# Performance work log

Measured on AMD Instinct MI355X. Metric: run time of the kernel, lower is better.

Reference implementation:

```python
import jax, jax.numpy as jnp
import numpy as np
import math

N = 100000   # nodes
E = 1600000  # edges
H = 64       # hidden_dim
TD = 32      # time_dim
B = 8        # number of graphs in batch

def _lin(key, din, dout):
    kw, kb = jax.random.split(key)
    s = 1.0 / math.sqrt(din)
    return (jax.random.uniform(kw, (din, dout), jnp.float32, -s, s),
            jax.random.uniform(kb, (dout,), jnp.float32, -s, s))

def setup_inputs() -> dict:
    key = jax.random.key(0)
    ks = jax.random.split(key, 20)
    inp = {}
    inp['condition'] = jax.random.normal(ks[0], (N, 6), jnp.float32)
    inp['edge_attr'] = jax.random.normal(ks[1], (E, 2), jnp.float32)
    inp['edge_index'] = jax.random.randint(ks[2], (2, E), 0, N, jnp.int64 if jax.config.jax_enable_x64 else jnp.int32)
    inp['batch'] = jnp.sort(jax.random.randint(ks[3], (N,), 0, B))
    # node_mlp: 7->H->H
    inp['w_n1'], inp['b_n1'] = _lin(ks[4], 7, H)
    inp['w_n2'], inp['b_n2'] = _lin(ks[5], H, H)
    # edge_mlp: 2->H->H
    inp['w_e1'], inp['b_e1'] = _lin(ks[6], 2, H)
    inp['w_e2'], inp['b_e2'] = _lin(ks[7], H, H)
    # time_mlp: SiLU -> Linear(TD,H)
    inp['w_t'], inp['b_t'] = _lin(ks[8], TD, H)
    # three GINEConv inner MLPs: H->H->H each
    inp['w_c1a'], inp['b_c1a'] = _lin(ks[9], H, H)
    inp['w_c1b'], inp['b_c1b'] = _lin(ks[10], H, H)
    inp['w_c2a'], inp['b_c2a'] = _lin(ks[11], H, H)
    inp['w_c2b'], inp['b_c2b'] = _lin(ks[12], H, H)
    inp['w_c3a'], inp['b_c3a'] = _lin(ks[13], H, H)
    inp['w_c3b'], inp['b_c3b'] = _lin(ks[14], H, H)
    # final_mlp: H->H->1
    inp['w_f1'], inp['b_f1'] = _lin(ks[15], H, H)
    inp['w_f2'], inp['b_f2'] = _lin(ks[16], H, 1)
    return inp

def _mlp2(x, w1, b1, w2, b2):
    return jax.nn.silu(x @ w1 + b1) @ w2 + b2

def _time_emb(t, dim):
    half = dim // 2
    freqs = jnp.exp(jnp.arange(half, dtype=jnp.float32) * (-math.log(10000.0) / (half - 1)))
    ang = t[:, None].astype(jnp.float32) * freqs[None, :]
    return jnp.concatenate([jnp.sin(ang), jnp.cos(ang)], axis=-1)

def _gine_conv(h, ef, src, dst, w1, b1, w2, b2):
    # GINEConv (eps=0): nn(x_i + sum_j relu(x_j + edge_attr))
    msg = jax.nn.relu(h[src] + ef)                       # [E,H]
    agg = jax.ops.segment_sum(msg, dst, num_segments=N)  # [N,H]
    return _mlp2(h + agg, w1, b1, w2, b2)

def reference(condition, edge_attr,
              w_n1, b_n1, w_n2, b_n2,
              w_e1, b_e1, w_e2, b_e2,
              w_t, b_t,
              w_c1a, b_c1a, w_c1b, b_c1b,
              w_c2a, b_c2a, w_c2b, b_c2b,
              w_c3a, b_c3a, w_c3b, b_c3b,
              w_f1, b_f1, w_f2, b_f2,
              edge_index, batch):
    n = condition.shape[0]
    x_in = jnp.concatenate([jnp.zeros((n, 1), condition.dtype), condition], axis=-1)  # [N,7]
    h = _mlp2(x_in, w_n1, b_n1, w_n2, b_n2)          # [N,H]
    ef = _mlp2(edge_attr, w_e1, b_e1, w_e2, b_e2)    # [E,H]
    # t = zeros(batch_size) as in original; batch_size = B (static)
    t_emb = _time_emb(jnp.zeros((B,), jnp.float32), TD)   # [B,TD]
    t_feat = jax.nn.silu(t_emb) @ w_t + b_t               # [B,H]
    h = h + t_feat[batch]
    src, dst = edge_index[0], edge_index[1]
    h = jax.nn.silu(_gine_conv(h, ef, src, dst, w_c1a, b_c1a, w_c1b, b_c1b))
    h = jax.nn.silu(_gine_conv(h, ef, src, dst, w_c2a, b_c2a, w_c2b, b_c2b))
    h = jax.nn.silu(_gine_conv(h, ef, src, dst, w_c3a, b_c3a, w_c3b, b_c3b))
    return _mlp2(h, w_f1, b_f1, w_f2, b_f2)          # [N,1]
```

## Files before the change

kernel.cpp:

```cpp
#include <hip/hip_runtime.h>
#include <hip/hip_bf16.h>

#define NN 100000
#define NE 1600000
#define SCAN_BLOCKS 98

typedef short short8 __attribute__((ext_vector_type(8)));
typedef float floatx4 __attribute__((ext_vector_type(4)));

__device__ __forceinline__ float silu_f(float x){ return x / (1.0f + __expf(-x)); }

__device__ __forceinline__ unsigned short f2bf(float x) {
    __hip_bfloat16 h = __float2bfloat16(x);
    unsigned short u; __builtin_memcpy(&u, &h, 2); return u;
}
__device__ __forceinline__ float bf2f(unsigned short u) {
    return __uint_as_float((unsigned)u << 16);
}

__device__ __forceinline__ float dot64(const float* vec, const float* wrow) {
    float ax = 0.f, ay = 0.f, az = 0.f, aw = 0.f;
#pragma unroll
    for (int k = 0; k < 64; k += 4) {
        float4 w = *(const float4*)(wrow + k);
        float4 v = *(const float4*)(vec + k);
        ax = fmaf(v.x, w.x, ax); ay = fmaf(v.y, w.y, ay);
        az = fmaf(v.z, w.z, az); aw = fmaf(v.w, w.w, aw);
    }
    return (ax + ay) + (az + aw);
}
__device__ __forceinline__ void load_wT(const float* __restrict__ w, float* s, int t) {
    for (int i = t; i < 4096; i += 256) { int k = i >> 6, j = i & 63; s[j * 68 + k] = w[i]; }
}

__global__ void tvec_kernel(const float* __restrict__ w_t, const float* __restrict__ b_t,
                            float* __restrict__ tvec) {
    int j = threadIdx.x;
    const float s1 = 0.7310585786300049f;
    float acc = b_t[j];
#pragma unroll
    for (int i = 16; i < 32; ++i) acc = fmaf(s1, w_t[i * 64 + j], acc);
    tvec[j] = acc;
}

__global__ __launch_bounds__(256) void node_init_kernel(
    const float* __restrict__ cond,
    const float* __restrict__ w1, const float* __restrict__ b1,
    const float* __restrict__ w2, const float* __restrict__ b2,
    const float* __restrict__ tvec,
    float* __restrict__ h, float* __restrict__ agg)
{
    __shared__ float s_w1[6 * 64];
    __shared__ float s_w2t[64 * 68];
    __shared__ float s_b1[64], s_b2[64];
    __shared__ float s_hid[4][64];
    int t = threadIdx.x;
    for (int i = t; i < 384; i += 256) s_w1[i] = w1[64 + i];
    load_wT(w2, s_w2t, t);
    if (t < 64) { s_b1[t] = b1[t]; s_b2[t] = b2[t] + tvec[t]; }
    __syncthreads();
    int lane = t & 63, grp = t >> 6;
    const int groups = (NN + 3) >> 2;
    for (int g = blockIdx.x; g < groups; g += gridDim.x) {
        int n = (g << 2) + grp;
        if (n < NN) {
            float acc = s_b1[lane];
#pragma unroll
            for (int i = 0; i < 6; ++i) acc = fmaf(cond[n * 6 + i], s_w1[i * 64 + lane], acc);
            s_hid[grp][lane] = silu_f(acc);
            float o = s_b2[lane] + dot64(s_hid[grp], s_w2t + lane * 68);
            size_t off = (size_t)n * 64 + lane;
            h[off] = o;
            if (agg) agg[off] = 0.f;
        }
    }
}

__global__ __launch_bounds__(256) void zero_kernel(int* __restrict__ p, int n) {
    int i = blockIdx.x * 256 + threadIdx.x;
    if (i < n) p[i] = 0;
}
__global__ __launch_bounds__(256) void hist_kernel(const int* __restrict__ dst, int* __restrict__ cnt) {
    int e = blockIdx.x * 256 + threadIdx.x;
    if (e < NE) atomicAdd(&cnt[dst[e]], 1);
}
__global__ __launch_bounds__(256) void scan1_kernel(const int* __restrict__ cnt,
                                                    int* __restrict__ offs, int* __restrict__ bsum) {
    __shared__ int s_w[4];
    int t = threadIdx.x;
    int base = blockIdx.x * 1024 + t * 4;
    int v0 = (base + 0 < NN) ? cnt[base + 0] : 0;
    int v1 = (base + 1 < NN) ? cnt[base + 1] : 0;
    int v2 = (base + 2 < NN) ? cnt[base + 2] : 0;
    int v3 = (base + 3 < NN) ? cnt[base + 3] : 0;
    int tsum = v0 + v1 + v2 + v3;
    int lane = t & 63, w = t >> 6;
    int x = tsum;
#pragma unroll
    for (int d = 1; d < 64; d <<= 1) { int y = __shfl_up(x, d, 64); if (lane >= d) x += y; }
    if (lane == 63) s_w[w] = x;
    __syncthreads();
    if (t == 0) {
        int a = 0;
#pragma unroll
        for (int i = 0; i < 4; ++i) { int b = s_w[i]; s_w[i] = a; a += b; }
        bsum[blockIdx.x] = a;
    }
    __syncthreads();
    int excl = x - tsum + s_w[w];
    if (base + 0 < NN) offs[base + 0] = excl;
    if (base + 1 < NN) offs[base + 1] = excl + v0;
    if (base + 2 < NN) offs[base + 2] = excl + v0 + v1;
    if (base + 3 < NN) offs[base + 3] = excl + v0 + v1 + v2;
}
__global__ void scan2_kernel(const int* __restrict__ bsum, int* __restrict__ bscan, int nb) {
    __shared__ int s_w[2];
    int t = threadIdx.x;
    int v = (t < nb) ? bsum[t] : 0;
    int lane = t & 63, w = t >> 6;
    int x = v;
#pragma unroll
    for (int d = 1; d < 64; d <<= 1) { int y = __shfl_up(x, d, 64); if (lane >= d) x += y; }
    if (lane == 63) s_w[w] = x;
    __syncthreads();
    int add = (w == 1) ? s_w[0] : 0;
    if (t < nb) bscan[t] = x - v + add;
}
__global__ __launch_bounds__(256) void scan3_kernel(int* __restrict__ offs,
                                                    const int* __restrict__ bscan,
                                                    int* __restrict__ cursor) {
    int i = blockIdx.x * 256 + threadIdx.x;
    if (i < NN) {
        int v = offs[i] + bscan[i >> 10];
        offs[i] = v;
        cursor[i] = v;
    }
    if (i == 0) offs[NN] = NE;
}
__global__ __launch_bounds__(256) void scatter_pack_kernel(const int* __restrict__ dst,
                                                           const int* __restrict__ src,
                                                           const float* __restrict__ ea,
                                                           int* __restrict__ cursor,
                                                           int4* __restrict__ pack) {
    int e = blockIdx.x * 256 + threadIdx.x;
    if (e >= NE) return;
    float2 a = *(const float2*)(ea + (size_t)e * 2);
    int pos = atomicAdd(&cursor[dst[e]], 1);
    pack[pos] = make_int4(src[e], __float_as_int(a.x), __float_as_int(a.y), 0);
}
__global__ __launch_bounds__(256) void copy_src_kernel(const int4* __restrict__ pack,
                                                       int* __restrict__ srcc) {
    int i = blockIdx.x * 256 + threadIdx.x;
    if (i < NE) srcc[i] = pack[i].x;
}

__global__ __launch_bounds__(256, 2) void edge_feat_mfma_kernel(
    const int4* __restrict__ pack,
    const float* __restrict__ w1, const float* __restrict__ b1,
    const float* __restrict__ w2, const float* __restrict__ b2,
    __hip_bfloat16* __restrict__ ef)
{
    int t = threadIdx.x;
    int lane = t & 63, wv = t >> 6;
    int er = lane & 15;
    int kg = lane >> 4;
    float w1x[2][8], w1y[2][8], b1v[2][8];
#pragma unroll
    for (int c = 0; c < 2; ++c)
#pragma unroll
        for (int j = 0; j < 8; ++j) {
            int k = c * 32 + kg * 8 + j;
            w1x[c][j] = w1[k];
            w1y[c][j] = w1[64 + k];
            b1v[c][j] = b1[k];
        }
    short8 bfrag[2][4];
#pragma unroll
    for (int c = 0; c < 2; ++c)
#pragma unroll
        for (int tt = 0; tt < 4; ++tt)
#pragma unroll
            for (int j = 0; j < 8; ++j) {
                int k = c * 32 + kg * 8 + j;
                bfrag[c][tt][j] = (short)f2bf(w2[k * 64 + 4 * er + tt]);
            }
    float4 b2v = *(const float4*)(b2 + 4 * er);

    const int nchunk = NE / 16;
    for (int ch = blockIdx.x * 4 + wv; ch < nchunk; ch += gridDim.x * 4) {
        int i0 = ch * 16;
        int4 p = pack[i0 + er];
        float ax = __int_as_float(p.y), ay = __int_as_float(p.z);
        short8 afrag[2];
#pragma unroll
        for (int c = 0; c < 2; ++c)
#pragma unroll
            for (int j = 0; j < 8; ++j) {
                float hid = silu_f(fmaf(ax, w1x[c][j], fmaf(ay, w1y[c][j], b1v[c][j])));
                afrag[c][j] = (short)f2bf(hid);
            }
        floatx4 acc0 = {0,0,0,0}, acc1 = {0,0,0,0}, acc2 = {0,0,0,0}, acc3 = {0,0,0,0};
        acc0 = __builtin_amdgcn_mfma_f32_16x16x32_bf16(afrag[0], bfrag[0][0], acc0, 0, 0, 0);
        acc0 = __builtin_amdgcn_mfma_f32_16x16x32_bf16(afrag[1], bfrag[1][0], acc0, 0, 0, 0);
        acc1 = __builtin_amdgcn_mfma_f32_16x16x32_bf16(afrag[0], bfrag[0][1], acc1, 0, 0, 0);
        acc1 = __builtin_amdgcn_mfma_f32_16x16x32_bf16(afrag[1], bfrag[1][1], acc1, 0, 0, 0);
        acc2 = __builtin_amdgcn_mfma_f32_16x16x32_bf16(afrag[0], bfrag[0][2], acc2, 0, 0, 0);
        acc2 = __builtin_amdgcn_mfma_f32_16x16x32_bf16(afrag[1], bfrag[1][2], acc2, 0, 0, 0);
        acc3 = __builtin_amdgcn_mfma_f32_16x16x32_bf16(afrag[0], bfrag[0][3], acc3, 0, 0, 0);
        acc3 = __builtin_amdgcn_mfma_f32_16x16x32_bf16(afrag[1], bfrag[1][3], acc3, 0, 0, 0);
#pragma unroll
        for (int q = 0; q < 4; ++q) {
            ushort4 o;
            o.x = f2bf(acc0[q] + b2v.x);
            o.y = f2bf(acc1[q] + b2v.y);
            o.z = f2bf(acc2[q] + b2v.z);
            o.w = f2bf(acc3[q] + b2v.w);
            *(ushort4*)((unsigned short*)ef + (size_t)(i0 + kg * 4 + q) * 64 + 4 * er) = o;
        }
    }
}

__global__ __launch_bounds__(256) void agg_kernel(
    const float* __restrict__ hin, float* __restrict__ u,
    const int* __restrict__ offs, const int* __restrict__ srcc,
    const __hip_bfloat16* __restrict__ ef)
{
    int t = threadIdx.x, lane = t & 63, grp = t >> 6;
    int n = blockIdx.x * 4 + grp;
    if (n >= NN) return;
    size_t off = (size_t)n * 64 + lane;
    float acc = hin[off];
    const unsigned short* efu = (const unsigned short*)ef;
    int i0 = offs[n], i1 = offs[n + 1];
    for (int ib = i0; ib < i1; ib += 64) {
        int m = i1 - ib; if (m > 64) m = 64;
        int myS = 0;
        if (lane < m) myS = srcc[ib + lane];
        int j = 0;
        for (; j + 8 <= m; j += 8) {
            float hs[8], ev[8];
#pragma unroll
            for (int q = 0; q < 8; ++q) {
                int s = __shfl(myS, j + q, 64);
                hs[q] = hin[(size_t)s * 64 + lane];
                ev[q] = __uint_as_float((unsigned)efu[(size_t)(ib + j + q) * 64 + lane] << 16);
            }
#pragma unroll
            for (int q = 0; q < 8; ++q) acc += fmaxf(hs[q] + ev[q], 0.f);
        }
        for (; j < m; ++j) {
            int s = __shfl(myS, j, 64);
            float hs = hin[(size_t)s * 64 + lane];
            float ev = __uint_as_float((unsigned)efu[(size_t)(ib + j) * 64 + lane] << 16);
            acc += fmaxf(hs + ev, 0.f);
        }
    }
    u[off] = acc;
}

__global__ __launch_bounds__(256) void node_mlp_mfma_kernel(
    const float* __restrict__ u, float* __restrict__ h,
    const float* __restrict__ wa, const float* __restrict__ ba,
    const float* __restrict__ wb, const float* __restrict__ bb)
{
    __shared__ float s_hid[4][16 * 72];
    int t = threadIdx.x, lane = t & 63, wv = t >> 6;
    int er = lane & 15, kg = lane >> 4;
    short8 waH[2][4], waL[2][4], wbH[2][4], wbL[2][4];
#pragma unroll
    for (int c = 0; c < 2; ++c)
#pragma unroll
        for (int tt = 0; tt < 4; ++tt)
#pragma unroll
            for (int j = 0; j < 8; ++j) {
                int k = c * 32 + kg * 8 + j;
                float vA = wa[k * 64 + 4 * er + tt];
                unsigned short hA = f2bf(vA);
                waH[c][tt][j] = (short)hA;
                waL[c][tt][j] = (short)f2bf(vA - bf2f(hA));
                float vB = wb[k * 64 + 4 * er + tt];
                unsigned short hB = f2bf(vB);
                wbH[c][tt][j] = (short)hB;
                wbL[c][tt][j] = (short)f2bf(vB - bf2f(hB));
            }
    float4 bav = *(const float4*)(ba + 4 * er);
    float4 bbv = *(const float4*)(bb + 4 * er);
    float* hid = s_hid[wv];

    const int ntile = NN / 16;
    for (int tile = blockIdx.x * 4 + wv; tile < ntile; tile += gridDim.x * 4) {
        int i0 = tile * 16;
        short8 aH[2], aL[2];
#pragma unroll
        for (int c = 0; c < 2; ++c) {
            const float* up = u + (size_t)(i0 + er) * 64 + c * 32 + kg * 8;
            float4 u0 = *(const float4*)(up);
            float4 u1 = *(const float4*)(up + 4);
            float uv[8] = {u0.x, u0.y, u0.z, u0.w, u1.x, u1.y, u1.z, u1.w};
#pragma unroll
            for (int j = 0; j < 8; ++j) {
                unsigned short hi = f2bf(uv[j]);
                aH[c][j] = (short)hi;
                aL[c][j] = (short)f2bf(uv[j] - bf2f(hi));
            }
        }
        floatx4 acc[4] = {{0,0,0,0},{0,0,0,0},{0,0,0,0},{0,0,0,0}};
#pragma unroll
        for (int tt = 0; tt < 4; ++tt)
#pragma unroll
            for (int c = 0; c < 2; ++c) {
                acc[tt] = __builtin_amdgcn_mfma_f32_16x16x32_bf16(aH[c], waH[c][tt], acc[tt], 0, 0, 0);
                acc[tt] = __builtin_amdgcn_mfma_f32_16x16x32_bf16(aL[c], waH[c][tt], acc[tt], 0, 0, 0);
                acc[tt] = __builtin_amdgcn_mfma_f32_16x16x32_bf16(aH[c], waL[c][tt], acc[tt], 0, 0, 0);
            }
#pragma unroll
        for (int q = 0; q < 4; ++q) {
            float4 hv;
            hv.x = silu_f(acc[0][q] + bav.x);
            hv.y = silu_f(acc[1][q] + bav.y);
            hv.z = silu_f(acc[2][q] + bav.z);
            hv.w = silu_f(acc[3][q] + bav.w);
            *(float4*)(hid + (kg * 4 + q) * 72 + 4 * er) = hv;
        }
        short8 cH[2], cL[2];
#pragma unroll
        for (int c = 0; c < 2; ++c) {
            const float* hp = hid + er * 72 + c * 32 + kg * 8;
            float4 h0 = *(const float4*)(hp);
            float4 h1 = *(const float4*)(hp + 4);
            float hv[8] = {h0.x, h0.y, h0.z, h0.w, h1.x, h1.y, h1.z, h1.w};
#pragma unroll
            for (int j = 0; j < 8; ++j) {
                unsigned short hi = f2bf(hv[j]);
                cH[c][j] = (short)hi;
                cL[c][j] = (short)f2bf(hv[j] - bf2f(hi));
            }
        }
        floatx4 acc2[4] = {{0,0,0,0},{0,0,0,0},{0,0,0,0},{0,0,0,0}};
#pragma unroll
        for (int tt = 0; tt < 4; ++tt)
#pragma unroll
            for (int c = 0; c < 2; ++c) {
                acc2[tt] = __builtin_amdgcn_mfma_f32_16x16x32_bf16(cH[c], wbH[c][tt], acc2[tt], 0, 0, 0);
                acc2[tt] = __builtin_amdgcn_mfma_f32_16x16x32_bf16(cL[c], wbH[c][tt], acc2[tt], 0, 0, 0);
                acc2[tt] = __builtin_amdgcn_mfma_f32_16x16x32_bf16(cH[c], wbL[c][tt], acc2[tt], 0, 0, 0);
            }
#pragma unroll
        for (int q = 0; q < 4; ++q) {
            float4 ov;
            ov.x = silu_f(acc2[0][q] + bbv.x);
            ov.y = silu_f(acc2[1][q] + bbv.y);
            ov.z = silu_f(acc2[2][q] + bbv.z);
            ov.w = silu_f(acc2[3][q] + bbv.w);
            *(float4*)(h + (size_t)(i0 + kg * 4 + q) * 64 + 4 * er) = ov;
        }
    }
}

__global__ __launch_bounds__(256, 3) void edge_feat_fallback_kernel(
    const float* __restrict__ ea,
    const float* __restrict__ w1, const float* __restrict__ b1,
    const float* __restrict__ w2, const float* __restrict__ b2,
    __hip_bfloat16* __restrict__ ef)
{
    __shared__ float s_w1[128], s_b1[64], s_b2[64];
    __shared__ float s_hid[4][64];
    int t = threadIdx.x;
    if (t < 128) s_w1[t] = w1[t];
    if (t < 64) { s_b1[t] = b1[t]; s_b2[t] = b2[t]; }
    int lane = t & 63, grp = t >> 6;
    __syncthreads();
    const int groups = NE >> 2;
    for (int g = blockIdx.x; g < groups; g += gridDim.x) {
        int e = (g << 2) + grp;
        float2 a = *(const float2*)(ea + (size_t)e * 2);
        float acc = fmaf(a.x, s_w1[lane], fmaf(a.y, s_w1[64 + lane], s_b1[lane]));
        s_hid[grp][lane] = silu_f(acc);
        float o = s_b2[lane];
#pragma unroll
        for (int k = 0; k < 64; k += 4) {
            float4 v = *(const float4*)&s_hid[grp][k];
            o = fmaf(v.x, w2[(k+0)*64+lane], o);
            o = fmaf(v.y, w2[(k+1)*64+lane], o);
            o = fmaf(v.z, w2[(k+2)*64+lane], o);
            o = fmaf(v.w, w2[(k+3)*64+lane], o);
        }
        ef[(size_t)e * 64 + lane] = __float2bfloat16(o);
    }
}

__global__ __launch_bounds__(256) void msg_agg_kernel(
    const int* __restrict__ src, const int* __restrict__ dst,
    const float* __restrict__ h, const __hip_bfloat16* __restrict__ ef,
    float* __restrict__ agg)
{
    int tid = blockIdx.x * 256 + threadIdx.x;
    int e = tid >> 4;
    if (e >= NE) return;
    int q = tid & 15;
    int s = src[e], d = dst[e];
    float4 hv = *(const float4*)(h + (size_t)s * 64 + q * 4);
    ushort4 ev = *(const ushort4*)(ef + (size_t)e * 64 + q * 4);
    float m0 = fmaxf(hv.x + __uint_as_float((unsigned)ev.x << 16), 0.f);
    float m1 = fmaxf(hv.y + __uint_as_float((unsigned)ev.y << 16), 0.f);
    float m2 = fmaxf(hv.z + __uint_as_float((unsigned)ev.z << 16), 0.f);
    float m3 = fmaxf(hv.w + __uint_as_float((unsigned)ev.w << 16), 0.f);
    float* ap = agg + (size_t)d * 64 + q * 4;
    atomicAdd(ap + 0, m0); atomicAdd(ap + 1, m1);
    atomicAdd(ap + 2, m2); atomicAdd(ap + 3, m3);
}

__global__ __launch_bounds__(256) void node_update_kernel(
    float* __restrict__ h, float* __restrict__ agg,
    const float* __restrict__ wa, const float* __restrict__ ba,
    const float* __restrict__ wb, const float* __restrict__ bb)
{
    __shared__ float s_wat[64 * 68], s_wbt[64 * 68];
    __shared__ float s_ba[64], s_bb[64];
    __shared__ float s_u[4][64], s_hid[4][64];
    int t = threadIdx.x;
    load_wT(wa, s_wat, t);
    load_wT(wb, s_wbt, t);
    if (t < 64) { s_ba[t] = ba[t]; s_bb[t] = bb[t]; }
    __syncthreads();
    int lane = t & 63, grp = t >> 6;
    const int groups = (NN + 3) >> 2;
    for (int g = blockIdx.x; g < groups; g += gridDim.x) {
        int n = (g << 2) + grp;
        if (n < NN) {
            size_t off = (size_t)n * 64 + lane;
            float uv = h[off] + agg[off];
            agg[off] = 0.f;
            s_u[grp][lane] = uv;
            float hid = silu_f(s_ba[lane] + dot64(s_u[grp], s_wat + lane * 68));
            s_hid[grp][lane] = hid;
            float o = silu_f(s_bb[lane] + dot64(s_hid[grp], s_wbt + lane * 68));
            h[off] = o;
        }
    }
}

__global__ __launch_bounds__(256) void final_kernel(
    const float* __restrict__ hin,
    const float* __restrict__ w1, const float* __restrict__ b1,
    const float* __restrict__ w2, const float* __restrict__ b2,
    float* __restrict__ out)
{
    __shared__ float s_w1t[64 * 68];
    __shared__ float s_b1[64], s_w2[64];
    __shared__ float s_u[4][64];
    int t = threadIdx.x;
    load_wT(w1, s_w1t, t);
    if (t < 64) { s_b1[t] = b1[t]; s_w2[t] = w2[t]; }
    __syncthreads();
    int lane = t & 63, grp = t >> 6;
    float b2v = b2[0];
    const int groups = (NN + 3) >> 2;
    for (int g = blockIdx.x; g < groups; g += gridDim.x) {
        int n = (g << 2) + grp;
        if (n < NN) {
            s_u[grp][lane] = hin[(size_t)n * 64 + lane];
            float hid = silu_f(s_b1[lane] + dot64(s_u[grp], s_w1t + lane * 68));
            float v = hid * s_w2[lane];
#pragma unroll
            for (int off = 32; off; off >>= 1) v += __shfl_xor(v, off, 64);
            if (lane == 0) out[n] = v + b2v;
        }
    }
}

extern "C" void kernel_launch(void* const* d_in, const int* in_sizes, int n_in,
                              void* d_out, int out_size, void* d_ws, size_t ws_size,
                              hipStream_t stream) {
    const float* cond = (const float*)d_in[0];
    const float* ea   = (const float*)d_in[1];
    const int*   ei   = (const int*)d_in[2];
    const float* w_n1 = (const float*)d_in[4];  const float* b_n1 = (const float*)d_in[5];
    const float* w_n2 = (const float*)d_in[6];  const float* b_n2 = (const float*)d_in[7];
    const float* w_e1 = (const float*)d_in[8];  const float* b_e1 = (const float*)d_in[9];
    const float* w_e2 = (const float*)d_in[10]; const float* b_e2 = (const float*)d_in[11];
    const float* w_t  = (const float*)d_in[12]; const float* b_t  = (const float*)d_in[13];
    const float* wca[3] = {(const float*)d_in[14], (const float*)d_in[18], (const float*)d_in[22]};
    const float* bca[3] = {(const float*)d_in[15], (const float*)d_in[19], (const float*)d_in[23]};
    const float* wcb[3] = {(const float*)d_in[16], (const float*)d_in[20], (const float*)d_in[24]};
    const float* bcb[3] = {(const float*)d_in[17], (const float*)d_in[21], (const float*)d_in[25]};
    const float* w_f1 = (const float*)d_in[26]; const float* b_f1 = (const float*)d_in[27];
    const float* w_f2 = (const float*)d_in[28]; const float* b_f2 = (const float*)d_in[29];
    float* out = (float*)d_out;

    const int* srcp = ei;
    const int* dstp = ei + NE;
    char* ws = (char*)d_ws;

    size_t o = 0;
    float* tvec = (float*)(ws + o); o += 256;
    float* h    = (float*)(ws + o); o += (size_t)NN * 64 * 4;
    float* u    = (float*)(ws + o); o += (size_t)NN * 64 * 4;
    int* offs   = (int*)(ws + o);   o += ((size_t)(NN + 1) * 4 + 255) & ~255ULL;
    int* cnt    = (int*)(ws + o);   o += ((size_t)NN * 4 + 255) & ~255ULL;
    int* bsum   = (int*)(ws + o);   o += 512;
    int* bscan  = (int*)(ws + o);   o += 512;
    int* srcc   = (int*)(ws + o);   o += (size_t)NE * 4;
    __hip_bfloat16* ef = (__hip_bfloat16*)(ws + o); o += (size_t)NE * 64 * 2;
    const size_t REQ_A = o;
    int4* pack = (int4*)u;

    if (ws_size >= REQ_A) {
        hipLaunchKernelGGL(tvec_kernel, dim3(1), dim3(64), 0, stream, w_t, b_t, tvec);
        hipLaunchKernelGGL(zero_kernel, dim3((NN + 255) / 256), dim3(256), 0, stream, cnt, NN);
        hipLaunchKernelGGL(hist_kernel, dim3((NE + 255) / 256), dim3(256), 0, stream, dstp, cnt);
        hipLaunchKernelGGL(scan1_kernel, dim3(SCAN_BLOCKS), dim3(256), 0, stream, cnt, offs, bsum);
        hipLaunchKernelGGL(scan2_kernel, dim3(1), dim3(128), 0, stream, bsum, bscan, SCAN_BLOCKS);
        hipLaunchKernelGGL(scan3_kernel, dim3((NN + 255) / 256), dim3(256), 0, stream, offs, bscan, cnt);
        hipLaunchKernelGGL(scatter_pack_kernel, dim3((NE + 255) / 256), dim3(256), 0, stream,
                           dstp, srcp, ea, cnt, pack);
        hipLaunchKernelGGL(copy_src_kernel, dim3((NE + 255) / 256), dim3(256), 0, stream,
                           pack, srcc);
        hipLaunchKernelGGL(node_init_kernel, dim3(1024), dim3(256), 0, stream,
                           cond, w_n1, b_n1, w_n2, b_n2, tvec, h, (float*)nullptr);
        hipLaunchKernelGGL(edge_feat_mfma_kernel, dim3(2048), dim3(256), 0, stream,
                           pack, w_e1, b_e1, w_e2, b_e2, ef);
        for (int l = 0; l < 3; ++l) {
            hipLaunchKernelGGL(agg_kernel, dim3((NN + 3) / 4), dim3(256), 0, stream,
                               h, u, offs, srcc, ef);
            hipLaunchKernelGGL(node_mlp_mfma_kernel, dim3(391), dim3(256), 0, stream,
                               u, h, wca[l], bca[l], wcb[l], bcb[l]);
        }
        hipLaunchKernelGGL(final_kernel, dim3(1024), dim3(256), 0, stream,
                           h, w_f1, b_f1, w_f2, b_f2, out);
    } else {
        float* tvecB = (float*)ws;
        float* hB    = (float*)(ws + 256);
        float* agg   = hB + (size_t)NN * 64;
        __hip_bfloat16* efB = (__hip_bfloat16*)(agg + (size_t)NN * 64);
        hipLaunchKernelGGL(tvec_kernel, dim3(1), dim3(64), 0, stream, w_t, b_t, tvecB);
        hipLaunchKernelGGL(node_init_kernel, dim3(1024), dim3(256), 0, stream,
                           cond, w_n1, b_n1, w_n2, b_n2, tvecB, hB, agg);
        hipLaunchKernelGGL(edge_feat_fallback_kernel, dim3(1024), dim3(256), 0, stream,
                           ea, w_e1, b_e1, w_e2, b_e2, efB);
        for (int l = 0; l < 3; ++l) {
            hipLaunchKernelGGL(msg_agg_kernel, dim3((NE * 16) / 256), dim3(256), 0, stream,
                               srcp, dstp, hB, efB, agg);
            hipLaunchKernelGGL(node_update_kernel, dim3(1024), dim3(256), 0, stream,
                               hB, agg, wca[l], bca[l], wcb[l], bcb[l]);
        }
        hipLaunchKernelGGL(final_kernel, dim3(1024), dim3(256), 0, stream,
                           hB, w_f1, b_f1, w_f2, b_f2, out);
    }
}
```

Before: 640.9 us.

## Aggregate two nodes per wavefront with paired features and nontemporal edge loads

The aggregation kernel now maps each node to a half-wavefront of 32 lanes. Each lane handles two features, using float2 gathers of h and 32-bit loads of packed bf16 edge features, so each memory instruction moves more bytes and each wave covers twice as many nodes. Edge-feature and source-index streams use nontemporal loads, and the edge MLP writes its output with nontemporal stores, so these streamed data are meant to pollute the cache less and leave room for the reused h rows. The risk is longer per-lane serial chains and more divergence between the two nodes sharing a wave when their degrees differ.

```diff
diff --git a/kernel.cpp b/kernel.cpp
--- a/kernel.cpp
+++ b/kernel.cpp
@@ -7,6 +7,8 @@
 
 typedef short short8 __attribute__((ext_vector_type(8)));
 typedef float floatx4 __attribute__((ext_vector_type(4)));
+typedef int   intx4   __attribute__((ext_vector_type(4)));
+typedef unsigned short ushortx4 __attribute__((ext_vector_type(4)));
 
 __device__ __forceinline__ float silu_f(float x){ return x / (1.0f + __expf(-x)); }
 
@@ -141,21 +143,22 @@
                                                            const int* __restrict__ src,
                                                            const float* __restrict__ ea,
                                                            int* __restrict__ cursor,
-                                                           int4* __restrict__ pack) {
+                                                           intx4* __restrict__ pack) {
     int e = blockIdx.x * 256 + threadIdx.x;
     if (e >= NE) return;
     float2 a = *(const float2*)(ea + (size_t)e * 2);
     int pos = atomicAdd(&cursor[dst[e]], 1);
-    pack[pos] = make_int4(src[e], __float_as_int(a.x), __float_as_int(a.y), 0);
-}
-__global__ __launch_bounds__(256) void copy_src_kernel(const int4* __restrict__ pack,
+    intx4 p = { src[e], __float_as_int(a.x), __float_as_int(a.y), 0 };
+    pack[pos] = p;
+}
+__global__ __launch_bounds__(256) void copy_src_kernel(const intx4* __restrict__ pack,
                                                        int* __restrict__ srcc) {
     int i = blockIdx.x * 256 + threadIdx.x;
     if (i < NE) srcc[i] = pack[i].x;
 }
 
 __global__ __launch_bounds__(256, 2) void edge_feat_mfma_kernel(
-    const int4* __restrict__ pack,
+    const intx4* __restrict__ pack,
     const float* __restrict__ w1, const float* __restrict__ b1,
     const float* __restrict__ w2, const float* __restrict__ b2,
     __hip_bfloat16* __restrict__ ef)
@@ -189,7 +192,7 @@
     const int nchunk = NE / 16;
     for (int ch = blockIdx.x * 4 + wv; ch < nchunk; ch += gridDim.x * 4) {
         int i0 = ch * 16;
-        int4 p = pack[i0 + er];
+        intx4 p = __builtin_nontemporal_load(pack + i0 + er);
         float ax = __int_as_float(p.y), ay = __int_as_float(p.z);
         short8 afrag[2];
 #pragma unroll
@@ -210,12 +213,13 @@
         acc3 = __builtin_amdgcn_mfma_f32_16x16x32_bf16(afrag[1], bfrag[1][3], acc3, 0, 0, 0);
 #pragma unroll
         for (int q = 0; q < 4; ++q) {
-            ushort4 o;
+            ushortx4 o;
             o.x = f2bf(acc0[q] + b2v.x);
             o.y = f2bf(acc1[q] + b2v.y);
             o.z = f2bf(acc2[q] + b2v.z);
             o.w = f2bf(acc3[q] + b2v.w);
-            *(ushort4*)((unsigned short*)ef + (size_t)(i0 + kg * 4 + q) * 64 + 4 * er) = o;
+            __builtin_nontemporal_store(o,
+                (ushortx4*)((unsigned short*)ef + (size_t)(i0 + kg * 4 + q) * 64 + 4 * er));
         }
     }
 }
@@ -225,37 +229,43 @@
     const int* __restrict__ offs, const int* __restrict__ srcc,
     const __hip_bfloat16* __restrict__ ef)
 {
-    int t = threadIdx.x, lane = t & 63, grp = t >> 6;
-    int n = blockIdx.x * 4 + grp;
+    int t = threadIdx.x;
+    int lane = t & 63, wv = t >> 6;
+    int half = lane >> 5, l32 = lane & 31;
+    int n = blockIdx.x * 8 + wv * 2 + half;
     if (n >= NN) return;
-    size_t off = (size_t)n * 64 + lane;
-    float acc = hin[off];
-    const unsigned short* efu = (const unsigned short*)ef;
+    size_t off = (size_t)n * 64 + l32 * 2;
+    float2 acc = *(const float2*)(hin + off);
+    const unsigned int* efu = (const unsigned int*)ef;
     int i0 = offs[n], i1 = offs[n + 1];
-    for (int ib = i0; ib < i1; ib += 64) {
-        int m = i1 - ib; if (m > 64) m = 64;
+    for (int ib = i0; ib < i1; ib += 32) {
+        int m = i1 - ib; if (m > 32) m = 32;
         int myS = 0;
-        if (lane < m) myS = srcc[ib + lane];
+        if (l32 < m) myS = __builtin_nontemporal_load(srcc + ib + l32);
         int j = 0;
         for (; j + 8 <= m; j += 8) {
-            float hs[8], ev[8];
+            float2 hs[8]; unsigned int ev[8];
 #pragma unroll
             for (int q = 0; q < 8; ++q) {
-                int s = __shfl(myS, j + q, 64);
-                hs[q] = hin[(size_t)s * 64 + lane];
-                ev[q] = __uint_as_float((unsigned)efu[(size_t)(ib + j + q) * 64 + lane] << 16);
-            }
-#pragma unroll
-            for (int q = 0; q < 8; ++q) acc += fmaxf(hs[q] + ev[q], 0.f);
+                int s = __shfl(myS, j + q, 32);
+                hs[q] = *(const float2*)(hin + (size_t)s * 64 + l32 * 2);
+                ev[q] = __builtin_nontemporal_load(efu + (size_t)(ib + j + q) * 32 + l32);
+            }
+#pragma unroll
+            for (int q = 0; q < 8; ++q) {
+                acc.x += fmaxf(hs[q].x + bf2f((unsigned short)(ev[q] & 0xffffu)), 0.f);
+                acc.y += fmaxf(hs[q].y + bf2f((unsigned short)(ev[q] >> 16)), 0.f);
+            }
         }
         for (; j < m; ++j) {
-            int s = __shfl(myS, j, 64);
-            float hs = hin[(size_t)s * 64 + lane];
-            float ev = __uint_as_float((unsigned)efu[(size_t)(ib + j) * 64 + lane] << 16);
-            acc += fmaxf(hs + ev, 0.f);
-        }
-    }
-    u[off] = acc;
+            int s = __shfl(myS, j, 32);
+            float2 hs = *(const float2*)(hin + (size_t)s * 64 + l32 * 2);
+            unsigned int ev = __builtin_nontemporal_load(efu + (size_t)(ib + j) * 32 + l32);
+            acc.x += fmaxf(hs.x + bf2f((unsigned short)(ev & 0xffffu)), 0.f);
+            acc.y += fmaxf(hs.y + bf2f((unsigned short)(ev >> 16)), 0.f);
+        }
+    }
+    *(float2*)(u + off) = acc;
 }
 
 __global__ __launch_bounds__(256) void node_mlp_mfma_kernel(
@@ -503,7 +513,7 @@
     int* srcc   = (int*)(ws + o);   o += (size_t)NE * 4;
     __hip_bfloat16* ef = (__hip_bfloat16*)(ws + o); o += (size_t)NE * 64 * 2;
     const size_t REQ_A = o;
-    int4* pack = (int4*)u;
+    intx4* pack = (intx4*)u;
 
     if (ws_size >= REQ_A) {
         hipLaunchKernelGGL(tvec_kernel, dim3(1), dim3(64), 0, stream, w_t, b_t, tvec);
@@ -521,7 +531,7 @@
         hipLaunchKernelGGL(edge_feat_mfma_kernel, dim3(2048), dim3(256), 0, stream,
                            pack, w_e1, b_e1, w_e2, b_e2, ef);
         for (int l = 0; l < 3; ++l) {
-            hipLaunchKernelGGL(agg_kernel, dim3((NN + 3) / 4), dim3(256), 0, stream,
+            hipLaunchKernelGGL(agg_kernel, dim3((NN + 7) / 8), dim3(256), 0, stream,
                                h, u, offs, srcc, ef);
             hipLaunchKernelGGL(node_mlp_mfma_kernel, dim3(391), dim3(256), 0, stream,
                                u, h, wca[l], bca[l], wcb[l], bcb[l]);
```

After: 670.9 us. 4.7% more time.
